# Kernel tuning notes

Hardware: AMD Instinct MI355X
Metric: run time of the kernel (lower is better)

Reference implementation:

```python
import jax, jax.numpy as jnp
import numpy as np

N = 50000        # nodes
E = 1600000      # edges
D_IN = 128       # input feature size
H = 4            # attention heads
C = 16           # hidden_size1 (per-head out channels)
HC = H * C       # 64
HS2 = 64         # hidden_size2
EDGE_DIM = 4
EPS = 1e-5


def setup_inputs() -> dict:
    key = jax.random.key(0)
    ks = jax.random.split(key, 64)
    inp = {}
    inp["data_x"] = jax.random.normal(ks[0], (N, D_IN), jnp.float32)
    inp["data_edge_index"] = jax.random.randint(ks[1], (2, E), 0, N)
    inp["data_edge_attr"] = jax.random.normal(ks[2], (E, EDGE_DIM), jnp.float32)
    i = 3
    s = 0.1
    for l, din in enumerate([D_IN, HC]):
        inp[f"Wl{l}"] = jax.random.normal(ks[i], (din, HC), jnp.float32) * s; i += 1
        inp[f"bl{l}"] = jnp.zeros((HC,), jnp.float32)
        inp[f"Wr{l}"] = jax.random.normal(ks[i], (din, HC), jnp.float32) * s; i += 1
        inp[f"br{l}"] = jnp.zeros((HC,), jnp.float32)
        inp[f"We{l}"] = jax.random.normal(ks[i], (EDGE_DIM, HC), jnp.float32) * s; i += 1
        inp[f"att{l}"] = jax.random.normal(ks[i], (H, C), jnp.float32) * s; i += 1
        inp[f"bias{l}"] = jnp.zeros((HC,), jnp.float32)
        inp[f"g{l}"] = jnp.ones((HC,), jnp.float32)
        inp[f"be{l}"] = jnp.zeros((HC,), jnp.float32)
    inp["W1"] = jax.random.normal(ks[i], (HC, HS2), jnp.float32) * s; i += 1
    inp["b1"] = jnp.zeros((HS2,), jnp.float32)
    inp["gf"] = jnp.ones((HS2,), jnp.float32)
    inp["bf"] = jnp.zeros((HS2,), jnp.float32)
    inp["W2"] = jax.random.normal(ks[i], (HS2, 1), jnp.float32) * s; i += 1
    inp["b2"] = jnp.zeros((1,), jnp.float32)
    return inp


def batch_norm(x, g, b):
    mu = x.mean(0)
    var = x.var(0)  # biased variance, matching torch BN normalization
    return (x - mu) * jax.lax.rsqrt(var + EPS) * g + b


def gatv2_layer(x, src, dst, eattr, Wl, bl, Wr, br, We, att, bias):
    # GATv2Conv, add_self_loops=False, concat=True, negative_slope=0.2
    n = x.shape[0]
    xl = (x @ Wl + bl).reshape(n, H, C)   # source transform (x_j side)
    xr = (x @ Wr + br).reshape(n, H, C)   # destination transform (x_i side)
    e = (eattr @ We).reshape(-1, H, C)    # edge-feature transform
    m = xl[src] + xr[dst] + e             # [E,H,C]
    m = jnp.where(m > 0, m, 0.2 * m)      # LeakyReLU(0.2)
    a = jnp.einsum('ehc,hc->eh', m, att)  # attention logits [E,H]
    amax = jax.ops.segment_max(a, dst, num_segments=n)   # per-dst max
    a = jnp.exp(a - amax[dst])
    asum = jax.ops.segment_sum(a, dst, num_segments=n)
    alpha = a / (asum[dst] + 1e-16)       # per-destination softmax
    out = jax.ops.segment_sum(xl[src] * alpha[:, :, None], dst, num_segments=n)
    return out.reshape(n, HC) + bias


def reference(data_x, data_edge_index, data_edge_attr,
              Wl0, bl0, Wr0, br0, We0, att0, bias0, g0, be0,
              Wl1, bl1, Wr1, br1, We1, att1, bias1, g1, be1,
              W1, b1, gf, bf, W2, b2):
    src = data_edge_index[0]
    dst = data_edge_index[1]
    layers = [(Wl0, bl0, Wr0, br0, We0, att0, bias0, g0, be0),
              (Wl1, bl1, Wr1, br1, We1, att1, bias1, g1, be1)]
    x = data_x
    for (Wl, bl, Wr, br, We, att, bias, g, be) in layers:
        x = gatv2_layer(x, src, dst, data_edge_attr, Wl, bl, Wr, br, We, att, bias)
        x = jax.nn.elu(batch_norm(x, g, be))
    x = x @ W1 + b1
    x = jax.nn.elu(batch_norm(x, gf, bf))
    return 5.0 * jnp.tanh(x @ W2 + b2)
```

## Files before the change

### kernel.cpp

```cpp
#include <hip/hip_runtime.h>
#include <hip/hip_bf16.h>
#include <cmath>

#define HC 64
typedef __hip_bfloat16 bf16;
typedef unsigned int uint;

__device__ __forceinline__ uint pack_bf2(float a, float b) {
    __hip_bfloat162 h = __float22bfloat162_rn(make_float2(a, b));
    return *reinterpret_cast<uint*>(&h);
}


__global__ __launch_bounds__(512) void bucket_hist_k(const int* __restrict__ dst,
                                                     int* __restrict__ bcnt, int E, int nbk) {
    __shared__ int lh[512];
    int t = threadIdx.x;
    for (int i = t; i < nbk; i += 512) lh[i] = 0;
    __syncthreads();
    int base = blockIdx.x * 8192;
#pragma unroll
    for (int k = 0; k < 16; ++k) {
        int e = base + k * 512 + t;
        if (e < E) atomicAdd(&lh[dst[e] >> 7], 1);
    }
    __syncthreads();
    for (int i = t; i < nbk; i += 512) if (lh[i]) atomicAdd(&bcnt[i], lh[i]);
}


__global__ __launch_bounds__(512) void bucket_scan_k(const int* __restrict__ bcnt,
                                                     int* __restrict__ bstart,
                                                     int* __restrict__ bcur, int nbk, int E) {
    __shared__ int tmp[512];
    int t = threadIdx.x;
    int v = (t < nbk) ? bcnt[t] : 0;
    tmp[t] = v;
    __syncthreads();
    for (int off = 1; off < 512; off <<= 1) {
        int a = (t >= off) ? tmp[t - off] : 0;
        __syncthreads();
        tmp[t] += a;
        __syncthreads();
    }
    if (t < nbk) { int ex = tmp[t] - v; bstart[t] = ex; bcur[t] = ex; }
    if (t == 0) bstart[nbk] = E;
}


__global__ __launch_bounds__(1024) void bucketA_k(
        const int* __restrict__ src, const int* __restrict__ dst,
        const float4* __restrict__ eattr, int* __restrict__ bcur,
        uint* __restrict__ tsd, uint2* __restrict__ tea, int E, int nbk) {
    __shared__ int lcnt[512];
    __shared__ int lbase[512];
    int t = threadIdx.x;
    for (int i = t; i < nbk; i += 1024) lcnt[i] = 0;
    __syncthreads();
    int base = blockIdx.x * 8192;
    int myb[8], mylp[8];
#pragma unroll
    for (int k = 0; k < 8; ++k) {
        int e = base + k * 1024 + t;
        if (e < E) {
            int b = dst[e] >> 7;
            myb[k] = b;
            mylp[k] = atomicAdd(&lcnt[b], 1);
        } else myb[k] = -1;
    }
    __syncthreads();
    for (int i = t; i < nbk; i += 1024) {
        int cc = lcnt[i];
        lbase[i] = cc ? atomicAdd(&bcur[i], cc) : 0;
    }
    __syncthreads();
#pragma unroll
    for (int k = 0; k < 8; ++k) {
        int e = base + k * 1024 + t;
        if (e >= E) continue;
        int pos = lbase[myb[k]] + mylp[k];
        int d = dst[e];
        tsd[pos] = (uint)src[e] | ((uint)(d & 127) << 25);
        float4 ea = eattr[e];
        tea[pos] = make_uint2(pack_bf2(ea.x, ea.y), pack_bf2(ea.z, ea.w));
    }
}


__global__ __launch_bounds__(256) void bucket_sort_k(
        const uint* __restrict__ tsd, const uint2* __restrict__ tea,
        const int* __restrict__ bstart,
        uint* __restrict__ src_sorted, uint2* __restrict__ eat_sorted,
        int* __restrict__ row_start, int n) {
    __shared__ int cnt[128], pfx[128], cur[128];
    int b = blockIdx.x, t = threadIdx.x;
    int i0 = bstart[b], i1 = bstart[b + 1];
    int node0 = b << 7;
    if (t < 128) cnt[t] = 0;
    __syncthreads();
    for (int i = i0 + t; i < i1; i += 256) atomicAdd(&cnt[tsd[i] >> 25], 1);
    __syncthreads();
    if (t < 128) pfx[t] = cnt[t];
    __syncthreads();
    for (int off = 1; off < 128; off <<= 1) {
        int a = (t < 128 && t >= off) ? pfx[t - off] : 0;
        __syncthreads();
        if (t < 128) pfx[t] += a;
        __syncthreads();
    }
    if (t < 128) {
        int ex = pfx[t] - cnt[t];
        cur[t] = ex;
        if (node0 + t <= n) row_start[node0 + t] = i0 + ex;
    }
    __syncthreads();
    for (int i = i0 + t; i < i1; i += 256) {
        uint u = tsd[i];
        int dl = (int)(u >> 25);
        int pos = i0 + atomicAdd(&cur[dl], 1);
        src_sorted[pos] = u & 0x1FFFFFFu;
        eat_sorted[pos] = tea[i];
    }
}


__global__ __launch_bounds__(256) void lin128_k(
        const float* __restrict__ x, int n,
        const float* __restrict__ Wl, const float* __restrict__ bl,
        const float* __restrict__ Wr, const float* __restrict__ br,
        bf16* __restrict__ xl, bf16* __restrict__ xr, int ngroups16) {
    __shared__ float2 sWl2[64 * 64];
    __shared__ float2 sWr2[64 * 64];
    __shared__ float sx[16 * 128];
    int t = threadIdx.x;
    for (int i = t; i < 64 * 64; i += 256) {
        int k2 = i >> 6, c = i & 63;
        sWl2[i] = make_float2(Wl[(2 * k2) * 64 + c], Wl[(2 * k2 + 1) * 64 + c]);
        sWr2[i] = make_float2(Wr[(2 * k2) * 64 + c], Wr[(2 * k2 + 1) * 64 + c]);
    }
    int c = t & 63, w = t >> 6;
    float blc = bl[c], brc = br[c];
    for (int gidx = blockIdx.x; gidx < ngroups16; gidx += gridDim.x) {
        int node0 = gidx * 16;
        __syncthreads();
        for (int i = t; i < 16 * 128; i += 256) {
            int r = node0 + (i >> 7);
            sx[i] = (r < n) ? x[(size_t)r * 128 + (i & 127)] : 0.f;
        }
        __syncthreads();
        float al0 = blc, al1 = blc, al2 = blc, al3 = blc;
        float ar0 = brc, ar1 = brc, ar2 = brc, ar3 = brc;
        const float* sx0 = sx + w * 4 * 128;
#pragma unroll 8
        for (int k2 = 0; k2 < 64; ++k2) {
            float2 wl = sWl2[k2 * 64 + c], wr = sWr2[k2 * 64 + c];
            float2 xa = *(const float2*)&sx0[k2 * 2];
            float2 xb = *(const float2*)&sx0[128 + k2 * 2];
            float2 xc = *(const float2*)&sx0[256 + k2 * 2];
            float2 xd = *(const float2*)&sx0[384 + k2 * 2];
            al0 = fmaf(xa.x, wl.x, al0); al0 = fmaf(xa.y, wl.y, al0);
            ar0 = fmaf(xa.x, wr.x, ar0); ar0 = fmaf(xa.y, wr.y, ar0);
            al1 = fmaf(xb.x, wl.x, al1); al1 = fmaf(xb.y, wl.y, al1);
            ar1 = fmaf(xb.x, wr.x, ar1); ar1 = fmaf(xb.y, wr.y, ar1);
            al2 = fmaf(xc.x, wl.x, al2); al2 = fmaf(xc.y, wl.y, al2);
            ar2 = fmaf(xc.x, wr.x, ar2); ar2 = fmaf(xc.y, wr.y, ar2);
            al3 = fmaf(xd.x, wl.x, al3); al3 = fmaf(xd.y, wl.y, al3);
            ar3 = fmaf(xd.x, wr.x, ar3); ar3 = fmaf(xd.y, wr.y, ar3);
        }
        int nb_ = node0 + w * 4;
        if (nb_ + 0 < n) { xl[(size_t)(nb_ + 0) * 64 + c] = __float2bfloat16(al0); xr[(size_t)(nb_ + 0) * 64 + c] = __float2bfloat16(ar0); }
        if (nb_ + 1 < n) { xl[(size_t)(nb_ + 1) * 64 + c] = __float2bfloat16(al1); xr[(size_t)(nb_ + 1) * 64 + c] = __float2bfloat16(ar1); }
        if (nb_ + 2 < n) { xl[(size_t)(nb_ + 2) * 64 + c] = __float2bfloat16(al2); xr[(size_t)(nb_ + 2) * 64 + c] = __float2bfloat16(ar2); }
        if (nb_ + 3 < n) { xl[(size_t)(nb_ + 3) * 64 + c] = __float2bfloat16(al3); xr[(size_t)(nb_ + 3) * 64 + c] = __float2bfloat16(ar3); }
    }
}


__global__ __launch_bounds__(256) void lin64bn_k(
        const float* __restrict__ x, int n,
        const float* __restrict__ sums, const float* __restrict__ sqs,
        const float* __restrict__ g, const float* __restrict__ be,
        const float* __restrict__ Wl, const float* __restrict__ bl,
        const float* __restrict__ Wr, const float* __restrict__ br,
        bf16* __restrict__ xl, bf16* __restrict__ xr, int ngroups16) {
    __shared__ float2 sWl2[32 * 64];
    __shared__ float2 sWr2[32 * 64];
    __shared__ float sx[16 * 64];
    __shared__ float ssc[64], ssh[64];
    int t = threadIdx.x;
    if (t < 64) {
        float inv_n = 1.f / n;
        float mu = sums[t] * inv_n;
        float var = sqs[t] * inv_n - mu * mu;
        float sc = rsqrtf(var + 1e-5f) * g[t];
        ssc[t] = sc; ssh[t] = be[t] - mu * sc;
    }
    for (int i = t; i < 32 * 64; i += 256) {
        int k2 = i >> 6, c = i & 63;
        sWl2[i] = make_float2(Wl[(2 * k2) * 64 + c], Wl[(2 * k2 + 1) * 64 + c]);
        sWr2[i] = make_float2(Wr[(2 * k2) * 64 + c], Wr[(2 * k2 + 1) * 64 + c]);
    }
    int c = t & 63, w = t >> 6;
    float blc = bl[c], brc = br[c];
    for (int gidx = blockIdx.x; gidx < ngroups16; gidx += gridDim.x) {
        int node0 = gidx * 16;
        __syncthreads();
        for (int i = t; i < 16 * 64; i += 256) {
            int r = node0 + (i >> 6);
            float v = (r < n) ? x[(size_t)r * 64 + (i & 63)] : 0.f;
            v = v * ssc[i & 63] + ssh[i & 63];
            sx[i] = v > 0.f ? v : __expf(v) - 1.f;
        }
        __syncthreads();
        float al0 = blc, al1 = blc, al2 = blc, al3 = blc;
        float ar0 = brc, ar1 = brc, ar2 = brc, ar3 = brc;
        const float* sx0 = sx + w * 4 * 64;
#pragma unroll 8
        for (int k2 = 0; k2 < 32; ++k2) {
            float2 wl = sWl2[k2 * 64 + c], wr = sWr2[k2 * 64 + c];
            float2 xa = *(const float2*)&sx0[k2 * 2];
            float2 xb = *(const float2*)&sx0[64 + k2 * 2];
            float2 xc = *(const float2*)&sx0[128 + k2 * 2];
            float2 xd = *(const float2*)&sx0[192 + k2 * 2];
            al0 = fmaf(xa.x, wl.x, al0); al0 = fmaf(xa.y, wl.y, al0);
            ar0 = fmaf(xa.x, wr.x, ar0); ar0 = fmaf(xa.y, wr.y, ar0);
            al1 = fmaf(xb.x, wl.x, al1); al1 = fmaf(xb.y, wl.y, al1);
            ar1 = fmaf(xb.x, wr.x, ar1); ar1 = fmaf(xb.y, wr.y, ar1);
            al2 = fmaf(xc.x, wl.x, al2); al2 = fmaf(xc.y, wl.y, al2);
            ar2 = fmaf(xc.x, wr.x, ar2); ar2 = fmaf(xc.y, wr.y, ar2);
            al3 = fmaf(xd.x, wl.x, al3); al3 = fmaf(xd.y, wl.y, al3);
            ar3 = fmaf(xd.x, wr.x, ar3); ar3 = fmaf(xd.y, wr.y, ar3);
        }
        int nb_ = node0 + w * 4;
        if (nb_ + 0 < n) { xl[(size_t)(nb_ + 0) * 64 + c] = __float2bfloat16(al0); xr[(size_t)(nb_ + 0) * 64 + c] = __float2bfloat16(ar0); }
        if (nb_ + 1 < n) { xl[(size_t)(nb_ + 1) * 64 + c] = __float2bfloat16(al1); xr[(size_t)(nb_ + 1) * 64 + c] = __float2bfloat16(ar1); }
        if (nb_ + 2 < n) { xl[(size_t)(nb_ + 2) * 64 + c] = __float2bfloat16(al2); xr[(size_t)(nb_ + 2) * 64 + c] = __float2bfloat16(ar2); }
        if (nb_ + 3 < n) { xl[(size_t)(nb_ + 3) * 64 + c] = __float2bfloat16(al3); xr[(size_t)(nb_ + 3) * 64 + c] = __float2bfloat16(ar3); }
    }
}


__global__ void gat_node_k(const bf16* __restrict__ xl, const bf16* __restrict__ xr,
                           const float* __restrict__ We, const float* __restrict__ att,
                           const int* __restrict__ row_start, const uint* __restrict__ src_sorted,
                           const uint2* __restrict__ eat,
                           float* __restrict__ out, int n) {
    int t = threadIdx.x;
    int c = t & 63;
    int node = blockIdx.x * 4 + (t >> 6);
    if (node >= n) return;
    float w0 = We[c], w1 = We[64 + c], w2 = We[128 + c], w3 = We[192 + c];
    float ratt = att[c] * 1.44269504f;
    float xrd = __bfloat162float(xr[((size_t)node << 6) + c]);
    int rs = row_start[node], re = row_start[node + 1];
    float srun = 0.f, acc = 0.f;

#define EDGE(U, EA, XV, M) { \
        float2 e01 = __bfloat1622float2(*reinterpret_cast<const __hip_bfloat162*>(&(EA).x)); \
        float2 e23 = __bfloat1622float2(*reinterpret_cast<const __hip_bfloat162*>(&(EA).y)); \
        float M = (XV) + xrd; \
        M = fmaf(e01.x, w0, M); M = fmaf(e01.y, w1, M); \
        M = fmaf(e23.x, w2, M); M = fmaf(e23.y, w3, M); \
        M = fmaxf(M, 0.2f * M); \
        M *= ratt; \
        M += __shfl_xor(M, 1); M += __shfl_xor(M, 2); \
        M += __shfl_xor(M, 4); M += __shfl_xor(M, 8); \
        float p = exp2f(M); \
        srun += p; \
        acc = fmaf(p, (XV), acc); \
    }

    int i = rs;
    for (; i + 4 <= re; i += 4) {
        uint u0 = src_sorted[i],     u1 = src_sorted[i + 1];
        uint u2 = src_sorted[i + 2], u3 = src_sorted[i + 3];
        uint2 e0 = eat[i],     e1 = eat[i + 1];
        uint2 e2 = eat[i + 2], e3 = eat[i + 3];
        float x0 = __bfloat162float(xl[((size_t)u0 << 6) + c]);
        float x1 = __bfloat162float(xl[((size_t)u1 << 6) + c]);
        float x2 = __bfloat162float(xl[((size_t)u2 << 6) + c]);
        float x3 = __bfloat162float(xl[((size_t)u3 << 6) + c]);
        EDGE(u0, e0, x0, m0); EDGE(u1, e1, x1, m1);
        EDGE(u2, e2, x2, m2); EDGE(u3, e3, x3, m3);
    }
    for (; i < re; ++i) {
        uint u0 = src_sorted[i];
        uint2 e0 = eat[i];
        float x0 = __bfloat162float(xl[((size_t)u0 << 6) + c]);
        EDGE(u0, e0, x0, m0);
    }
#undef EDGE

    out[((size_t)node << 6) + c] = acc / (srun + 1e-16f);
}


__global__ void bn_stats_k(const float* __restrict__ x, float* __restrict__ sums,
                           float* __restrict__ sqs, int n) {
    __shared__ float ls[256], lq[256];
    int t = threadIdx.x;
    int c = t & 63, sub = t >> 6;
    float s = 0.f, q = 0.f;
    for (int r = blockIdx.x * 4 + sub; r < n; r += gridDim.x * 4) {
        float v = x[(size_t)r * 64 + c];
        s += v;
        q = fmaf(v, v, q);
    }
    ls[t] = s; lq[t] = q;
    __syncthreads();
    if (t < 128) { ls[t] += ls[t + 128]; lq[t] += lq[t + 128]; }
    __syncthreads();
    if (t < 64) {
        atomicAdd(&sums[c], ls[t] + ls[t + 64]);
        atomicAdd(&sqs[c], lq[t] + lq[t + 64]);
    }
}


__global__ __launch_bounds__(256) void lin1_k(
        const float* __restrict__ x, int n,
        const float* __restrict__ sums, const float* __restrict__ sqs,
        const float* __restrict__ g, const float* __restrict__ be,
        const float* __restrict__ W, const float* __restrict__ b,
        float* __restrict__ y, float* __restrict__ sums_o, float* __restrict__ sqs_o,
        int ngroups16) {
    __shared__ float2 sW2[32 * 64];
    __shared__ float sx[16 * 64];
    __shared__ float ssc[64], ssh[64];
    __shared__ float ls[256], lq[256];
    int t = threadIdx.x;
    if (t < 64) {
        float inv_n = 1.f / n;
        float mu = sums[t] * inv_n;
        float var = sqs[t] * inv_n - mu * mu;
        float sc = rsqrtf(var + 1e-5f) * g[t];
        ssc[t] = sc; ssh[t] = be[t] - mu * sc;
    }
    for (int i = t; i < 32 * 64; i += 256) {
        int k2 = i >> 6, c = i & 63;
        sW2[i] = make_float2(W[(2 * k2) * 64 + c], W[(2 * k2 + 1) * 64 + c]);
    }
    int c = t & 63, w = t >> 6;
    float bc = b[c];
    float s = 0.f, q = 0.f;
    for (int gidx = blockIdx.x; gidx < ngroups16; gidx += gridDim.x) {
        int node0 = gidx * 16;
        __syncthreads();
        for (int i = t; i < 16 * 64; i += 256) {
            int r = node0 + (i >> 6);
            float v = (r < n) ? x[(size_t)r * 64 + (i & 63)] : 0.f;
            v = v * ssc[i & 63] + ssh[i & 63];
            sx[i] = v > 0.f ? v : __expf(v) - 1.f;
        }
        __syncthreads();
        float a0 = bc, a1 = bc, a2 = bc, a3 = bc;
        const float* sx0 = sx + w * 4 * 64;
#pragma unroll 8
        for (int k2 = 0; k2 < 32; ++k2) {
            float2 wv = sW2[k2 * 64 + c];
            float2 xa = *(const float2*)&sx0[k2 * 2];
            float2 xb = *(const float2*)&sx0[64 + k2 * 2];
            float2 xc = *(const float2*)&sx0[128 + k2 * 2];
            float2 xd = *(const float2*)&sx0[192 + k2 * 2];
            a0 = fmaf(xa.x, wv.x, a0); a0 = fmaf(xa.y, wv.y, a0);
            a1 = fmaf(xb.x, wv.x, a1); a1 = fmaf(xb.y, wv.y, a1);
            a2 = fmaf(xc.x, wv.x, a2); a2 = fmaf(xc.y, wv.y, a2);
            a3 = fmaf(xd.x, wv.x, a3); a3 = fmaf(xd.y, wv.y, a3);
        }
        int nb_ = node0 + w * 4;
        if (nb_ + 0 < n) { y[(size_t)(nb_ + 0) * 64 + c] = a0; s += a0; q = fmaf(a0, a0, q); }
        if (nb_ + 1 < n) { y[(size_t)(nb_ + 1) * 64 + c] = a1; s += a1; q = fmaf(a1, a1, q); }
        if (nb_ + 2 < n) { y[(size_t)(nb_ + 2) * 64 + c] = a2; s += a2; q = fmaf(a2, a2, q); }
        if (nb_ + 3 < n) { y[(size_t)(nb_ + 3) * 64 + c] = a3; s += a3; q = fmaf(a3, a3, q); }
    }
    __syncthreads();
    ls[t] = s; lq[t] = q;
    __syncthreads();
    if (t < 64) {
        float ss = ls[t] + ls[t + 64] + ls[t + 128] + ls[t + 192];
        float qq = lq[t] + lq[t + 64] + lq[t + 128] + lq[t + 192];
        atomicAdd(&sums_o[t], ss);
        atomicAdd(&sqs_o[t], qq);
    }
}


__global__ void final_k(const float* __restrict__ z, int n,
                        const float* __restrict__ sums, const float* __restrict__ sqs,
                        const float* __restrict__ g, const float* __restrict__ be,
                        const float* __restrict__ W2, const float* __restrict__ b2,
                        float* __restrict__ out) {
    int t = blockIdx.x * blockDim.x + threadIdx.x;
    int node = t >> 6, c = t & 63;
    if (node >= n) return;
    float inv_n = 1.f / n;
    float mu = sums[c] * inv_n;
    float var = sqs[c] * inv_n - mu * mu;
    float scc = rsqrtf(var + 1e-5f) * g[c];
    float sh = be[c] - mu * scc;
    float v = z[(size_t)node * 64 + c] * scc + sh;
    v = v > 0.f ? v : __expf(v) - 1.f;
    v *= W2[c];
    v += __shfl_xor(v, 1);
    v += __shfl_xor(v, 2);
    v += __shfl_xor(v, 4);
    v += __shfl_xor(v, 8);
    v += __shfl_xor(v, 16);
    v += __shfl_xor(v, 32);
    if (c == 0) out[node] = 5.0f * tanhf(v + b2[0]);
}


extern "C" void kernel_launch(void* const* d_in, const int* in_sizes, int n_in,
                              void* d_out, int out_size, void* d_ws, size_t ws_size,
                              hipStream_t stream) {
    const float* x0    = (const float*)d_in[0];
    const int*   eidx  = (const int*)d_in[1];
    const float* eattr = (const float*)d_in[2];

    const float* Wl[2]; const float* bl[2]; const float* Wr[2]; const float* br[2];
    const float* We[2]; const float* att[2]; const float* g[2]; const float* be[2];
    for (int l = 0; l < 2; ++l) {
        int base = 3 + l * 9;
        Wl[l]  = (const float*)d_in[base + 0];
        bl[l]  = (const float*)d_in[base + 1];
        Wr[l]  = (const float*)d_in[base + 2];
        br[l]  = (const float*)d_in[base + 3];
        We[l]  = (const float*)d_in[base + 4];
        att[l] = (const float*)d_in[base + 5];
        g[l]   = (const float*)d_in[base + 7];
        be[l]  = (const float*)d_in[base + 8];
    }
    const float* W1 = (const float*)d_in[21];
    const float* b1 = (const float*)d_in[22];
    const float* gf = (const float*)d_in[23];
    const float* bf = (const float*)d_in[24];
    const float* W2 = (const float*)d_in[25];
    const float* b2 = (const float*)d_in[26];

    const int N = in_sizes[0] / 128;
    const int E = in_sizes[1] / 2;
    const int* src = eidx;
    const int* dst = eidx + E;
    const int nbk = (N + 127) >> 7;

    float* ws = (float*)d_ws;
    size_t o = 0;
    float* regionA = ws + o; o += (size_t)2 * N * HC;
    uint2* tea = (uint2*)regionA;
    uint*  tsd = (uint*)(regionA + (size_t)2 * E);
    float* h0  = regionA;
    float* h1  = regionA + (size_t)N * HC;
    uint2* eat_sorted = (uint2*)(ws + o); o += (size_t)E * 2;
    uint*  src_sorted = (uint*)(ws + o);  o += (size_t)E;
    bf16*  xl  = (bf16*)(ws + o);  o += (size_t)N * 32;
    bf16*  xr  = (bf16*)(ws + o);  o += (size_t)N * 32;
    int*   row_start = (int*)(ws + o); o += (size_t)N + 1;
    int*   bcnt   = (int*)(ws + o); o += 512;
    int*   bstart = (int*)(ws + o); o += 513;
    int*   bcur   = (int*)(ws + o); o += 512;
    float* stats  = ws + o; o += 6 * HC;
    float* s0 = stats,        *q0 = stats + 64;
    float* s1 = stats + 128,  *q1 = stats + 192;
    float* sf = stats + 256,  *qf = stats + 320;

    const int ngroups4  = (N + 3) / 4;
    const int ngroups16 = (N + 15) / 16;
    const int EB = (E + 8191) / 8192;

    hipMemsetAsync(bcnt, 0, 512 * 4, stream);
    hipMemsetAsync(stats, 0, 6 * HC * 4, stream);

    bucket_hist_k<<<EB, 512, 0, stream>>>(dst, bcnt, E, nbk);
    bucket_scan_k<<<1, 512, 0, stream>>>(bcnt, bstart, bcur, nbk, E);
    bucketA_k<<<EB, 1024, 0, stream>>>(src, dst, (const float4*)eattr, bcur, tsd, tea, E, nbk);
    bucket_sort_k<<<nbk, 256, 0, stream>>>(tsd, tea, bstart, src_sorted, eat_sorted,
                                           row_start, N);

    lin128_k<<<512, 256, 0, stream>>>(x0, N, Wl[0], bl[0], Wr[0], br[0], xl, xr, ngroups16);
    gat_node_k<<<ngroups4, 256, 0, stream>>>(xl, xr, We[0], att[0], row_start,
                                             src_sorted, eat_sorted, h0, N);
    bn_stats_k<<<256, 256, 0, stream>>>(h0, s0, q0, N);

    lin64bn_k<<<512, 256, 0, stream>>>(h0, N, s0, q0, g[0], be[0],
                                       Wl[1], bl[1], Wr[1], br[1], xl, xr, ngroups16);
    gat_node_k<<<ngroups4, 256, 0, stream>>>(xl, xr, We[1], att[1], row_start,
                                             src_sorted, eat_sorted, h1, N);
    bn_stats_k<<<256, 256, 0, stream>>>(h1, s1, q1, N);

    float* y = h0;
    lin1_k<<<512, 256, 0, stream>>>(h1, N, s1, q1, g[1], be[1], W1, b1, y, sf, qf, ngroups16);
    final_k<<<(int)(((size_t)N * 64 + 255) / 256), 256, 0, stream>>>(
        y, N, sf, qf, gf, bf, W2, b2, (float*)d_out);
}
```

Baseline: 424.8 us.

## Process two edges per wavefront with two channels per lane in GAT aggregation

The per-node GAT kernel now splits each 64-lane wavefront into two halves. Each half handles a different edge, and each lane covers two channels using packed bf16 loads of 4 bytes. The sort stage stores byte offsets (src<<7) directly, which removes address arithmetic in the gather. The per-head reduction shrinks to three shuffles, and the two halves are combined at the end with a cross-half shuffle. This halves the number of serial edge iterations per node and widens the gather loads, at the cost of extra shuffles and a masked tail loop.

```diff
diff --git a/kernel.cpp b/kernel.cpp
--- a/kernel.cpp
+++ b/kernel.cpp
@@ -5,11 +5,14 @@
 #define HC 64
 typedef __hip_bfloat16 bf16;
 typedef unsigned int uint;
+typedef float v2f __attribute__((ext_vector_type(2)));
 
 __device__ __forceinline__ uint pack_bf2(float a, float b) {
     __hip_bfloat162 h = __float22bfloat162_rn(make_float2(a, b));
     return *reinterpret_cast<uint*>(&h);
 }
+__device__ __forceinline__ float bfl(uint u) { return __uint_as_float(u << 16); }
+__device__ __forceinline__ float bfh(uint u) { return __uint_as_float(u & 0xffff0000u); }
 
 
 __global__ __launch_bounds__(512) void bucket_hist_k(const int* __restrict__ dst,
@@ -90,7 +93,7 @@
 __global__ __launch_bounds__(256) void bucket_sort_k(
         const uint* __restrict__ tsd, const uint2* __restrict__ tea,
         const int* __restrict__ bstart,
-        uint* __restrict__ src_sorted, uint2* __restrict__ eat_sorted,
+        uint* __restrict__ spre_sorted, uint2* __restrict__ eat_sorted,
         int* __restrict__ row_start, int n) {
     __shared__ int cnt[128], pfx[128], cur[128];
     int b = blockIdx.x, t = threadIdx.x;
@@ -118,7 +121,7 @@
         uint u = tsd[i];
         int dl = (int)(u >> 25);
         int pos = i0 + atomicAdd(&cur[dl], 1);
-        src_sorted[pos] = u & 0x1FFFFFFu;
+        spre_sorted[pos] = (u & 0x1FFFFFFu) << 7;
         eat_sorted[pos] = tea[i];
     }
 }
@@ -240,58 +243,92 @@
 }
 
 
-__global__ void gat_node_k(const bf16* __restrict__ xl, const bf16* __restrict__ xr,
-                           const float* __restrict__ We, const float* __restrict__ att,
-                           const int* __restrict__ row_start, const uint* __restrict__ src_sorted,
-                           const uint2* __restrict__ eat,
-                           float* __restrict__ out, int n) {
-    int t = threadIdx.x;
-    int c = t & 63;
+__global__ __launch_bounds__(256) void gat_node_k(
+        const bf16* __restrict__ xl, const bf16* __restrict__ xr,
+        const float* __restrict__ We, const float* __restrict__ att,
+        const int* __restrict__ row_start, const uint* __restrict__ spre,
+        const uint2* __restrict__ eat,
+        float* __restrict__ out, int n) {
+    int t = threadIdx.x;
+    int lane = t & 63;
+    int half = lane >> 5;
+    int c2 = lane & 31;
     int node = blockIdx.x * 4 + (t >> 6);
     if (node >= n) return;
-    float w0 = We[c], w1 = We[64 + c], w2 = We[128 + c], w3 = We[192 + c];
-    float ratt = att[c] * 1.44269504f;
-    float xrd = __bfloat162float(xr[((size_t)node << 6) + c]);
+    int c0 = c2 << 1;
+    v2f w0 = {We[c0], We[c0 + 1]};
+    v2f w1 = {We[64 + c0], We[64 + c0 + 1]};
+    v2f w2 = {We[128 + c0], We[128 + c0 + 1]};
+    v2f w3 = {We[192 + c0], We[192 + c0 + 1]};
+    v2f ratt = {att[c0] * 1.44269504f, att[c0 + 1] * 1.44269504f};
+    const char* xlb = (const char*)xl;
+    uint xru = *(const uint*)((const char*)xr + ((size_t)node << 7) + ((uint)c0 << 1));
+    v2f xrd = {bfl(xru), bfh(xru)};
     int rs = row_start[node], re = row_start[node + 1];
-    float srun = 0.f, acc = 0.f;
-
-#define EDGE(U, EA, XV, M) { \
-        float2 e01 = __bfloat1622float2(*reinterpret_cast<const __hip_bfloat162*>(&(EA).x)); \
-        float2 e23 = __bfloat1622float2(*reinterpret_cast<const __hip_bfloat162*>(&(EA).y)); \
-        float M = (XV) + xrd; \
-        M = fmaf(e01.x, w0, M); M = fmaf(e01.y, w1, M); \
-        M = fmaf(e23.x, w2, M); M = fmaf(e23.y, w3, M); \
-        M = fmaxf(M, 0.2f * M); \
-        M *= ratt; \
-        M += __shfl_xor(M, 1); M += __shfl_xor(M, 2); \
-        M += __shfl_xor(M, 4); M += __shfl_xor(M, 8); \
-        float p = exp2f(M); \
-        srun += p; \
-        acc = fmaf(p, (XV), acc); \
+    v2f acc = {0.f, 0.f};
+    float srun = 0.f;
+    uint coff = (uint)c2 << 2;
+
+#define PROC(EA, XU, P) { \
+        v2f xv = {bfl(XU), bfh(XU)}; \
+        v2f z = xv + xrd; \
+        float e0 = bfl((EA).x), e1 = bfh((EA).x); \
+        float e2 = bfl((EA).y), e3 = bfh((EA).y); \
+        z.x = fmaf(e0, w0.x, z.x); z.y = fmaf(e0, w0.y, z.y); \
+        z.x = fmaf(e1, w1.x, z.x); z.y = fmaf(e1, w1.y, z.y); \
+        z.x = fmaf(e2, w2.x, z.x); z.y = fmaf(e2, w2.y, z.y); \
+        z.x = fmaf(e3, w3.x, z.x); z.y = fmaf(e3, w3.y, z.y); \
+        z = __builtin_elementwise_max(z, 0.2f * z); \
+        float v = fmaf(z.y, ratt.y, z.x * ratt.x); \
+        v += __shfl_xor(v, 1); v += __shfl_xor(v, 2); v += __shfl_xor(v, 4); \
+        float P = exp2f(v); \
+        srun += P; \
+        acc.x = fmaf(P, xv.x, acc.x); \
+        acc.y = fmaf(P, xv.y, acc.y); \
     }
 
     int i = rs;
     for (; i + 4 <= re; i += 4) {
-        uint u0 = src_sorted[i],     u1 = src_sorted[i + 1];
-        uint u2 = src_sorted[i + 2], u3 = src_sorted[i + 3];
-        uint2 e0 = eat[i],     e1 = eat[i + 1];
-        uint2 e2 = eat[i + 2], e3 = eat[i + 3];
-        float x0 = __bfloat162float(xl[((size_t)u0 << 6) + c]);
-        float x1 = __bfloat162float(xl[((size_t)u1 << 6) + c]);
-        float x2 = __bfloat162float(xl[((size_t)u2 << 6) + c]);
-        float x3 = __bfloat162float(xl[((size_t)u3 << 6) + c]);
-        EDGE(u0, e0, x0, m0); EDGE(u1, e1, x1, m1);
-        EDGE(u2, e2, x2, m2); EDGE(u3, e3, x3, m3);
-    }
-    for (; i < re; ++i) {
-        uint u0 = src_sorted[i];
-        uint2 e0 = eat[i];
-        float x0 = __bfloat162float(xl[((size_t)u0 << 6) + c]);
-        EDGE(u0, e0, x0, m0);
-    }
-#undef EDGE
-
-    out[((size_t)node << 6) + c] = acc / (srun + 1e-16f);
+        uint spA = spre[i + half], spB = spre[i + 2 + half];
+        uint2 eaA = eat[i + half], eaB = eat[i + 2 + half];
+        uint xuA = *(const uint*)(xlb + spA + coff);
+        uint xuB = *(const uint*)(xlb + spB + coff);
+        PROC(eaA, xuA, pA);
+        PROC(eaB, xuB, pB);
+    }
+    for (; i < re; i += 2) {
+        int ei = i + half;
+        bool ok = ei < re;
+        int eic = ok ? ei : i;
+        uint sp = spre[eic];
+        uint2 ea = eat[eic];
+        uint xu = *(const uint*)(xlb + sp + coff);
+        v2f xv = {bfl(xu), bfh(xu)};
+        v2f z = xv + xrd;
+        float e0 = bfl(ea.x), e1 = bfh(ea.x);
+        float e2 = bfl(ea.y), e3 = bfh(ea.y);
+        z.x = fmaf(e0, w0.x, z.x); z.y = fmaf(e0, w0.y, z.y);
+        z.x = fmaf(e1, w1.x, z.x); z.y = fmaf(e1, w1.y, z.y);
+        z.x = fmaf(e2, w2.x, z.x); z.y = fmaf(e2, w2.y, z.y);
+        z.x = fmaf(e3, w3.x, z.x); z.y = fmaf(e3, w3.y, z.y);
+        z = __builtin_elementwise_max(z, 0.2f * z);
+        float v = fmaf(z.y, ratt.y, z.x * ratt.x);
+        v += __shfl_xor(v, 1); v += __shfl_xor(v, 2); v += __shfl_xor(v, 4);
+        float p = ok ? exp2f(v) : 0.f;
+        srun += p;
+        acc.x = fmaf(p, xv.x, acc.x);
+        acc.y = fmaf(p, xv.y, acc.y);
+    }
+#undef PROC
+
+    srun += __shfl_xor(srun, 32);
+    acc.x += __shfl_xor(acc.x, 32);
+    acc.y += __shfl_xor(acc.y, 32);
+    if (half == 0) {
+        float inv = 1.f / (srun + 1e-16f);
+        float2 o = make_float2(acc.x * inv, acc.y * inv);
+        *(float2*)&out[((size_t)node << 6) + (uint)c0] = o;
+    }
 }
 
 
@@ -452,7 +489,7 @@
     float* h0  = regionA;
     float* h1  = regionA + (size_t)N * HC;
     uint2* eat_sorted = (uint2*)(ws + o); o += (size_t)E * 2;
-    uint*  src_sorted = (uint*)(ws + o);  o += (size_t)E;
+    uint*  spre_sorted = (uint*)(ws + o);  o += (size_t)E;
     bf16*  xl  = (bf16*)(ws + o);  o += (size_t)N * 32;
     bf16*  xr  = (bf16*)(ws + o);  o += (size_t)N * 32;
     int*   row_start = (int*)(ws + o); o += (size_t)N + 1;
@@ -474,18 +511,18 @@
     bucket_hist_k<<<EB, 512, 0, stream>>>(dst, bcnt, E, nbk);
     bucket_scan_k<<<1, 512, 0, stream>>>(bcnt, bstart, bcur, nbk, E);
     bucketA_k<<<EB, 1024, 0, stream>>>(src, dst, (const float4*)eattr, bcur, tsd, tea, E, nbk);
-    bucket_sort_k<<<nbk, 256, 0, stream>>>(tsd, tea, bstart, src_sorted, eat_sorted,
+    bucket_sort_k<<<nbk, 256, 0, stream>>>(tsd, tea, bstart, spre_sorted, eat_sorted,
                                            row_start, N);
 
     lin128_k<<<512, 256, 0, stream>>>(x0, N, Wl[0], bl[0], Wr[0], br[0], xl, xr, ngroups16);
     gat_node_k<<<ngroups4, 256, 0, stream>>>(xl, xr, We[0], att[0], row_start,
-                                             src_sorted, eat_sorted, h0, N);
+                                             spre_sorted, eat_sorted, h0, N);
     bn_stats_k<<<256, 256, 0, stream>>>(h0, s0, q0, N);
 
     lin64bn_k<<<512, 256, 0, stream>>>(h0, N, s0, q0, g[0], be[0],
                                        Wl[1], bl[1], Wr[1], br[1], xl, xr, ngroups16);
     gat_node_k<<<ngroups4, 256, 0, stream>>>(xl, xr, We[1], att[1], row_start,
-                                             src_sorted, eat_sorted, h1, N);
+                                             spre_sorted, eat_sorted, h1, N);
     bn_stats_k<<<256, 256, 0, stream>>>(h1, s1, q1, N);
 
     float* y = h0;
```

New measurement: 397.8 us. -6.4%, faster.
